# Optimization experiments

Measured on AMD Instinct MI355X. Metric: run time of the kernel, lower is better.

Reference implementation:

```python
import jax, jax.numpy as jnp
import numpy as np

I_DIM, H_DIM, O_DIM = 4, 8, 1


def setup_inputs() -> dict:
    key = jax.random.key(0)
    ks = jax.random.split(key, 7)
    B, T = 8192, 512
    s_ih = 1.0 / np.sqrt(H_DIM)
    x = jax.random.normal(ks[0], (B, T, I_DIM), dtype=jnp.float32)
    # PyTorch LSTM params: gate order i, f, g, o stacked along first axis (4H)
    W_ih = jax.random.uniform(ks[1], (4 * H_DIM, I_DIM), jnp.float32, -s_ih, s_ih)
    W_hh = jax.random.uniform(ks[2], (4 * H_DIM, H_DIM), jnp.float32, -s_ih, s_ih)
    b_ih = jax.random.uniform(ks[3], (4 * H_DIM,), jnp.float32, -s_ih, s_ih)
    b_hh = jax.random.uniform(ks[4], (4 * H_DIM,), jnp.float32, -s_ih, s_ih)
    W_fc = jax.random.uniform(ks[5], (O_DIM, H_DIM), jnp.float32, -s_ih, s_ih)
    b_fc = jax.random.uniform(ks[6], (O_DIM,), jnp.float32, -s_ih, s_ih)
    return {"x": x, "W_ih": W_ih, "W_hh": W_hh, "b_ih": b_ih, "b_hh": b_hh,
            "W_fc": W_fc, "b_fc": b_fc}


def _lstm_last_hidden(x, W_ih, W_hh, b_ih, b_hh):
    B, T, _ = x.shape
    H = W_hh.shape[1]
    # Precompute input projections for all timesteps: [B, T, 4H] -> [T, B, 4H]
    xg = jnp.einsum('bti,gi->btg', x, W_ih) + b_ih + b_hh
    xg = jnp.transpose(xg, (1, 0, 2))
    h0 = jnp.zeros((B, H), x.dtype)
    c0 = jnp.zeros((B, H), x.dtype)

    def step(carry, g_t):
        h, c = carry
        gates = g_t + h @ W_hh.T  # [B, 4H]
        i, f, g, o = jnp.split(gates, 4, axis=-1)
        i = jax.nn.sigmoid(i)
        f = jax.nn.sigmoid(f)
        g = jnp.tanh(g)
        o = jax.nn.sigmoid(o)
        c = f * c + i * g
        h = o * jnp.tanh(c)
        return (h, c), None

    (h_last, _), _ = jax.lax.scan(step, (h0, c0), xg)
    return h_last  # equals out[:, -1, :]


def reference(x, W_ih, W_hh, b_ih, b_hh, W_fc, b_fc):
    h_last = _lstm_last_hidden(x, W_ih, W_hh, b_ih, b_hh)
    return h_last @ W_fc.T + b_fc  # [B, output_dim]
```

## Files before the change

kernel.cpp:

```cpp
#include <hip/hip_runtime.h>

#define T_STEPS 512
#define CHUNK   32
#define NCHUNK  (T_STEPS / CHUNK)
#define EPB     32
#define ROWF    132
#define BUFF    (EPB * ROWF)
#define LOG2E   1.4426950408889634f

typedef float v2f __attribute__((ext_vector_type(2)));

__device__ __forceinline__ v2f pk_fma_b(v2f w, float s, v2f c) {
    v2f sv; sv.x = s;
    v2f d;
    asm("v_pk_fma_f32 %0, %1, %2, %3 op_sel_hi:[1,0,1]"
        : "=v"(d) : "v"(w), "v"(sv), "v"(c));
    return d;
}
__device__ __forceinline__ void pk_fma_acc(v2f& a, v2f w, float s) {
    v2f sv; sv.x = s;
    asm("v_pk_fma_f32 %0, %1, %2, %0 op_sel_hi:[1,0,1]"
        : "+v"(a) : "v"(w), "v"(sv));
}
__device__ __forceinline__ v2f pk_mul_b(v2f w, float s) {
    v2f sv; sv.x = s;
    v2f d;
    asm("v_pk_mul_f32 %0, %1, %2 op_sel_hi:[1,0]"
        : "=v"(d) : "v"(w), "v"(sv));
    return d;
}
__device__ __forceinline__ v2f pk_add2(v2f a, v2f b) {
    v2f d;
    asm("v_pk_add_f32 %0, %1, %2" : "=v"(d) : "v"(a), "v"(b));
    return d;
}

template <int CTRL>
__device__ __forceinline__ float dppf(float v) {
    return __int_as_float(__builtin_amdgcn_update_dpp(
        0, __float_as_int(v), CTRL, 0xF, 0xF, true));
}
template <int IMM>
__device__ __forceinline__ float swzf(float v) {
    return __int_as_float(__builtin_amdgcn_ds_swizzle(__float_as_int(v), IMM));
}

__global__ __launch_bounds__(256) void lstm_kernel(
    const float* __restrict__ x, const float* __restrict__ W_ih,
    const float* __restrict__ W_hh, const float* __restrict__ b_ih,
    const float* __restrict__ b_hh, const float* __restrict__ W_fc,
    const float* __restrict__ b_fc, float* __restrict__ out, int B)
{
    __shared__ float ldsx[2 * BUFF];

    const int tid = threadIdx.x;
    const int e   = tid >> 3;
    const int j   = tid & 7;

    const int ri = j, rf = 8 + j, rg = 16 + j, ro = 24 + j;
    v2f wihIF[4], wihGO[4], whhIF[8], whhGO[8], biasIF, biasGO;
    #pragma unroll
    for (int k = 0; k < 4; ++k) {
        wihIF[k] = v2f{W_ih[ri * 4 + k], W_ih[rf * 4 + k]};
        wihGO[k] = v2f{W_ih[rg * 4 + k], W_ih[ro * 4 + k]};
    }
    #pragma unroll
    for (int s = 0; s < 8; ++s) {
        const int m = j ^ s;
        whhIF[s] = v2f{W_hh[ri * 8 + m], W_hh[rf * 8 + m]};
        whhGO[s] = v2f{W_hh[rg * 8 + m], W_hh[ro * 8 + m]};
    }
    biasIF = v2f{b_ih[ri] + b_hh[ri], b_ih[rf] + b_hh[rf]};
    biasGO = v2f{b_ih[rg] + b_hh[rg], b_ih[ro] + b_hh[ro]};

    const int st  = tid & 31;
    const int se0 = tid >> 5;
    const float* gp0 = x + (size_t)(blockIdx.x * EPB + se0) * (T_STEPS * 4) + st * 4;
    const int wl0 = se0 * ROWF + st * 4;

    float4 v0, v1, v2, v3;
    v0 = *(const float4*)(gp0);
    v1 = *(const float4*)(gp0 + 8 * 2048);
    v2 = *(const float4*)(gp0 + 16 * 2048);
    v3 = *(const float4*)(gp0 + 24 * 2048);
    *(float4*)&ldsx[wl0 + 0 * 8 * ROWF] = v0;
    *(float4*)&ldsx[wl0 + 1 * 8 * ROWF] = v1;
    *(float4*)&ldsx[wl0 + 2 * 8 * ROWF] = v2;
    *(float4*)&ldsx[wl0 + 3 * 8 * ROWF] = v3;
    v0 = *(const float4*)(gp0 + CHUNK * 4);
    v1 = *(const float4*)(gp0 + CHUNK * 4 + 8 * 2048);
    v2 = *(const float4*)(gp0 + CHUNK * 4 + 16 * 2048);
    v3 = *(const float4*)(gp0 + CHUNK * 4 + 24 * 2048);
    __syncthreads();

    float h = 0.0f, c = 0.0f;
    const float nL  = -LOG2E;
    const float n2L = -2.0f * LOG2E;

    for (int n = 0; n < NCHUNK; ++n) {
        const int wb = ((n + 1) & 1) * BUFF + wl0;
        *(float4*)&ldsx[wb + 0 * 8 * ROWF] = v0;
        *(float4*)&ldsx[wb + 1 * 8 * ROWF] = v1;
        *(float4*)&ldsx[wb + 2 * 8 * ROWF] = v2;
        *(float4*)&ldsx[wb + 3 * 8 * ROWF] = v3;
        const int t2 = ((n + 2) & (NCHUNK - 1)) * (CHUNK * 4);
        v0 = *(const float4*)(gp0 + t2);
        v1 = *(const float4*)(gp0 + t2 + 8 * 2048);
        v2 = *(const float4*)(gp0 + t2 + 16 * 2048);
        v3 = *(const float4*)(gp0 + t2 + 24 * 2048);

        const float* xr = &ldsx[(n & 1) * BUFF + e * ROWF];
        float4 xc = *(const float4*)(xr);
        #pragma unroll
        for (int t = 0; t < CHUNK; ++t) {
            const float4 xn = *(const float4*)(xr + (((t + 1) & (CHUNK - 1)) * 4));
            const float4 xt = xc;

            const float s1 = dppf<0xB1>(h);
            const float s2 = dppf<0x4E>(h);
            const float s3 = dppf<0x1B>(h);
            const float s7 = dppf<0x141>(h);
            const float s4 = swzf<0x101F>(h);
            const float s5 = swzf<0x141F>(h);
            const float s6 = swzf<0x181F>(h);

            v2f aIF = pk_fma_b(wihIF[0], xt.x, biasIF);
            v2f bIF = pk_mul_b(wihIF[1], xt.y);
            v2f aGO = pk_fma_b(wihGO[0], xt.x, biasGO);
            v2f bGO = pk_mul_b(wihGO[1], xt.y);
            pk_fma_acc(aIF, wihIF[2], xt.z);  pk_fma_acc(bIF, wihIF[3], xt.w);
            pk_fma_acc(aGO, wihGO[2], xt.z);  pk_fma_acc(bGO, wihGO[3], xt.w);
            pk_fma_acc(aIF, whhIF[0], h);     pk_fma_acc(aGO, whhGO[0], h);
            pk_fma_acc(bIF, whhIF[1], s1);    pk_fma_acc(bGO, whhGO[1], s1);
            pk_fma_acc(aIF, whhIF[2], s2);    pk_fma_acc(aGO, whhGO[2], s2);
            pk_fma_acc(bIF, whhIF[3], s3);    pk_fma_acc(bGO, whhGO[3], s3);
            pk_fma_acc(aIF, whhIF[4], s4);    pk_fma_acc(aGO, whhGO[4], s4);
            pk_fma_acc(bIF, whhIF[5], s5);    pk_fma_acc(bGO, whhGO[5], s5);
            pk_fma_acc(aIF, whhIF[6], s6);    pk_fma_acc(aGO, whhGO[6], s6);
            pk_fma_acc(bIF, whhIF[7], s7);    pk_fma_acc(bGO, whhGO[7], s7);
            const v2f gIF = pk_add2(aIF, bIF);
            const v2f gGO = pk_add2(aGO, bGO);

            const float eI = __builtin_amdgcn_exp2f(nL  * gIF.x);
            const float eF = __builtin_amdgcn_exp2f(nL  * gIF.y);
            const float eG = __builtin_amdgcn_exp2f(n2L * gGO.x);
            const float eO = __builtin_amdgcn_exp2f(nL  * gGO.y);
            const float i_ = __builtin_amdgcn_rcpf(1.0f + eI);
            const float f_ = __builtin_amdgcn_rcpf(1.0f + eF);
            const float o_ = __builtin_amdgcn_rcpf(1.0f + eO);
            const float g_ = fmaf(__builtin_amdgcn_rcpf(1.0f + eG), 2.0f, -1.0f);

            c = fmaf(f_, c, i_ * g_);
            const float eC = __builtin_amdgcn_exp2f(n2L * c);
            h = o_ * fmaf(__builtin_amdgcn_rcpf(1.0f + eC), 2.0f, -1.0f);
            xc = xn;
        }
        __syncthreads();
    }

    float pr = h * W_fc[j];
    pr += __shfl_xor(pr, 1);
    pr += __shfl_xor(pr, 2);
    pr += __shfl_xor(pr, 4);
    if (j == 0) out[blockIdx.x * EPB + e] = pr + b_fc[0];
}

extern "C" void kernel_launch(void* const* d_in, const int* in_sizes, int n_in,
                              void* d_out, int out_size, void* d_ws, size_t ws_size,
                              hipStream_t stream) {
    const float* x    = (const float*)d_in[0];
    const float* W_ih = (const float*)d_in[1];
    const float* W_hh = (const float*)d_in[2];
    const float* b_ih = (const float*)d_in[3];
    const float* b_hh = (const float*)d_in[4];
    const float* W_fc = (const float*)d_in[5];
    const float* b_fc = (const float*)d_in[6];
    float* out = (float*)d_out;

    const int B = in_sizes[0] / (T_STEPS * 4);
    const int block = 256;
    const int grid = (B * 8) / block;
    lstm_kernel<<<grid, block, 0, stream>>>(x, W_ih, W_hh, b_ih, b_hh, W_fc, b_fc, out, B);
}
```

Before: 191.2 us.

## Fold exp scale into weights, merge reciprocals, hoist input projection off h chain

Pre-scales LSTM weights and biases by -log2e (or -2log2e for the g gate) so gate pre-activations feed exp2 directly. The cell state is kept in scaled form. The i*g and o*tanh(c) products are computed with a single shared reciprocal each, removing two rcp ops per step. The input projection is computed before the recurrent shuffles so it sits off the h-dependent critical path. Products of (1+e) terms may overflow to inf for large-magnitude gates, changing edge-case numerics.

```diff
diff --git a/kernel.cpp b/kernel.cpp
--- a/kernel.cpp
+++ b/kernel.cpp
@@ -57,21 +57,25 @@
     const int e   = tid >> 3;
     const int j   = tid & 7;
 
+    const float nL  = -LOG2E;
+    const float n2L = -2.0f * LOG2E;
+    const float P2L =  2.0f * LOG2E;
+
     const int ri = j, rf = 8 + j, rg = 16 + j, ro = 24 + j;
     v2f wihIF[4], wihGO[4], whhIF[8], whhGO[8], biasIF, biasGO;
     #pragma unroll
     for (int k = 0; k < 4; ++k) {
-        wihIF[k] = v2f{W_ih[ri * 4 + k], W_ih[rf * 4 + k]};
-        wihGO[k] = v2f{W_ih[rg * 4 + k], W_ih[ro * 4 + k]};
+        wihIF[k] = v2f{nL  * W_ih[ri * 4 + k], nL * W_ih[rf * 4 + k]};
+        wihGO[k] = v2f{n2L * W_ih[rg * 4 + k], nL * W_ih[ro * 4 + k]};
     }
     #pragma unroll
     for (int s = 0; s < 8; ++s) {
         const int m = j ^ s;
-        whhIF[s] = v2f{W_hh[ri * 8 + m], W_hh[rf * 8 + m]};
-        whhGO[s] = v2f{W_hh[rg * 8 + m], W_hh[ro * 8 + m]};
+        whhIF[s] = v2f{nL  * W_hh[ri * 8 + m], nL * W_hh[rf * 8 + m]};
+        whhGO[s] = v2f{n2L * W_hh[rg * 8 + m], nL * W_hh[ro * 8 + m]};
     }
-    biasIF = v2f{b_ih[ri] + b_hh[ri], b_ih[rf] + b_hh[rf]};
-    biasGO = v2f{b_ih[rg] + b_hh[rg], b_ih[ro] + b_hh[ro]};
+    biasIF = v2f{nL  * (b_ih[ri] + b_hh[ri]), nL * (b_ih[rf] + b_hh[rf])};
+    biasGO = v2f{n2L * (b_ih[rg] + b_hh[rg]), nL * (b_ih[ro] + b_hh[ro])};
 
     const int st  = tid & 31;
     const int se0 = tid >> 5;
@@ -93,9 +97,7 @@
     v3 = *(const float4*)(gp0 + CHUNK * 4 + 24 * 2048);
     __syncthreads();
 
-    float h = 0.0f, c = 0.0f;
-    const float nL  = -LOG2E;
-    const float n2L = -2.0f * LOG2E;
+    float h = 0.0f, ct = 0.0f;
 
     for (int n = 0; n < NCHUNK; ++n) {
         const int wb = ((n + 1) & 1) * BUFF + wl0;
@@ -116,6 +118,12 @@
             const float4 xn = *(const float4*)(xr + (((t + 1) & (CHUNK - 1)) * 4));
             const float4 xt = xc;
 
+            v2f xIF = pk_fma_b(wihIF[0], xt.x, biasIF);
+            v2f xGO = pk_fma_b(wihGO[0], xt.x, biasGO);
+            pk_fma_acc(xIF, wihIF[1], xt.y);  pk_fma_acc(xGO, wihGO[1], xt.y);
+            pk_fma_acc(xIF, wihIF[2], xt.z);  pk_fma_acc(xGO, wihGO[2], xt.z);
+            pk_fma_acc(xIF, wihIF[3], xt.w);  pk_fma_acc(xGO, wihGO[3], xt.w);
+
             const float s1 = dppf<0xB1>(h);
             const float s2 = dppf<0x4E>(h);
             const float s3 = dppf<0x1B>(h);
@@ -124,35 +132,32 @@
             const float s5 = swzf<0x141F>(h);
             const float s6 = swzf<0x181F>(h);
 
-            v2f aIF = pk_fma_b(wihIF[0], xt.x, biasIF);
-            v2f bIF = pk_mul_b(wihIF[1], xt.y);
-            v2f aGO = pk_fma_b(wihGO[0], xt.x, biasGO);
-            v2f bGO = pk_mul_b(wihGO[1], xt.y);
-            pk_fma_acc(aIF, wihIF[2], xt.z);  pk_fma_acc(bIF, wihIF[3], xt.w);
-            pk_fma_acc(aGO, wihGO[2], xt.z);  pk_fma_acc(bGO, wihGO[3], xt.w);
-            pk_fma_acc(aIF, whhIF[0], h);     pk_fma_acc(aGO, whhGO[0], h);
-            pk_fma_acc(bIF, whhIF[1], s1);    pk_fma_acc(bGO, whhGO[1], s1);
+            v2f aIF = pk_mul_b(whhIF[0], h);
+            v2f bIF = pk_mul_b(whhIF[1], s1);
+            v2f aGO = pk_mul_b(whhGO[0], h);
+            v2f bGO = pk_mul_b(whhGO[1], s1);
             pk_fma_acc(aIF, whhIF[2], s2);    pk_fma_acc(aGO, whhGO[2], s2);
             pk_fma_acc(bIF, whhIF[3], s3);    pk_fma_acc(bGO, whhGO[3], s3);
             pk_fma_acc(aIF, whhIF[4], s4);    pk_fma_acc(aGO, whhGO[4], s4);
             pk_fma_acc(bIF, whhIF[5], s5);    pk_fma_acc(bGO, whhGO[5], s5);
             pk_fma_acc(aIF, whhIF[6], s6);    pk_fma_acc(aGO, whhGO[6], s6);
             pk_fma_acc(bIF, whhIF[7], s7);    pk_fma_acc(bGO, whhGO[7], s7);
-            const v2f gIF = pk_add2(aIF, bIF);
-            const v2f gGO = pk_add2(aGO, bGO);
+            const v2f gIF = pk_add2(pk_add2(aIF, xIF), bIF);
+            const v2f gGO = pk_add2(pk_add2(aGO, xGO), bGO);
 
-            const float eI = __builtin_amdgcn_exp2f(nL  * gIF.x);
-            const float eF = __builtin_amdgcn_exp2f(nL  * gIF.y);
-            const float eG = __builtin_amdgcn_exp2f(n2L * gGO.x);
-            const float eO = __builtin_amdgcn_exp2f(nL  * gGO.y);
-            const float i_ = __builtin_amdgcn_rcpf(1.0f + eI);
+            const float eI = __builtin_amdgcn_exp2f(gIF.x);
+            const float eF = __builtin_amdgcn_exp2f(gIF.y);
+            const float eG = __builtin_amdgcn_exp2f(gGO.x);
+            const float eO = __builtin_amdgcn_exp2f(gGO.y);
+
+            const float R  = __builtin_amdgcn_rcpf((1.0f + eI) * (1.0f + eG));
             const float f_ = __builtin_amdgcn_rcpf(1.0f + eF);
-            const float o_ = __builtin_amdgcn_rcpf(1.0f + eO);
-            const float g_ = fmaf(__builtin_amdgcn_rcpf(1.0f + eG), 2.0f, -1.0f);
+            const float ign = fmaf(eG, P2L, n2L) * R;
+            ct = fmaf(f_, ct, ign);
+            const float eC = __builtin_amdgcn_exp2f(ct);
+            const float RC = __builtin_amdgcn_rcpf((1.0f + eO) * (1.0f + eC));
+            h = (1.0f - eC) * RC;
 
-            c = fmaf(f_, c, i_ * g_);
-            const float eC = __builtin_amdgcn_exp2f(n2L * c);
-            h = o_ * fmaf(__builtin_amdgcn_rcpf(1.0f + eC), 2.0f, -1.0f);
             xc = xn;
         }
         __syncthreads();
```

New measurement: 186.0 us. 1.03x faster.
